# Optimization experiments

Measured on AMD Instinct MI355X. Metric: run time of the kernel, lower is better.

The kernel has to match this reference:

```python
import jax, jax.numpy as jnp
import numpy as np

B, IN, HID, OUT, E, NMAP = 16384, 64, 128, 1, 64, 1000


def setup_inputs() -> dict:
    key = jax.random.key(0)
    ks = jax.random.split(key, 7)
    x = jax.random.normal(ks[0], (B, IN), dtype=jnp.float32)
    num = jax.random.randint(ks[1], (B,), 0, NMAP, dtype=jnp.int64)
    c = jax.random.randint(ks[2], (NMAP,), 0, E, dtype=jnp.int64)
    # per-expert 2-layer MLP params (kaiming-ish scale)
    W1 = jax.random.normal(ks[3], (E, IN, HID), dtype=jnp.float32) * (1.0 / np.sqrt(IN))
    b1 = jnp.zeros((E, HID), dtype=jnp.float32)
    W2 = jax.random.normal(ks[4], (E, HID, OUT), dtype=jnp.float32) * (1.0 / np.sqrt(HID))
    b2 = jnp.zeros((E, OUT), dtype=jnp.float32)
    return {"x": x, "num": num, "c": c, "W1": W1, "b1": b1, "W2": W2, "b2": b2}


def reference(x, num, c, W1, b1, W2, b2):
    # per-sample expert id: c[num[i]]
    e = c[num]                                   # [B]
    # gather each sample's expert weights and run batched MLP
    h = jnp.einsum('bi,bih->bh', x, W1[e]) + b1[e]   # [B, HID]
    h = jax.nn.relu(h)
    y = jnp.einsum('bh,bho->bo', h, W2[e]) + b2[e]   # [B, OUT]
    return jax.nn.sigmoid(y)
```

## Files before the change

kernel.cpp:

```cpp
#include <hip/hip_runtime.h>
#include <math.h>

#define B_N    16384
#define IN_D   64
#define HID_D  128
#define E_N    64
#define SB_N   64
#define CAP_BE 48
#define GRP    4
#define NGRP   (SB_N / GRP)
#define CAPC   (GRP * CAP_BE)

#define FRAG_OFF  0
#define FRAG_SZ   (E_N * IN_D * HID_D * 2)
#define CNT_OFF   (FRAG_OFF + FRAG_SZ)
#define CNT_SZ    (E_N * SB_N * 4)
#define LIST_OFF  (CNT_OFF + CNT_SZ)

typedef __attribute__((ext_vector_type(8))) short v8s;
typedef __attribute__((ext_vector_type(4))) float v4f;

__device__ __forceinline__ short f2bf(float f) {
    unsigned int u = __float_as_uint(f);
    u += 0x7fffu + ((u >> 16) & 1u);
    return (short)(u >> 16);
}

__global__ __launch_bounds__(256) void ka_prep(
    const int* __restrict__ num, const int* __restrict__ c,
    const float* __restrict__ W1, unsigned char* __restrict__ ws)
{
    const int tid = threadIdx.x;
    if (blockIdx.x < SB_N) {
        __shared__ int lcnt[E_N];
        __shared__ int llist[E_N * CAP_BE];
        int* cnt  = (int*)(ws + CNT_OFF);
        int* list = (int*)(ws + LIST_OFF);
        const int b = blockIdx.x;
        if (tid < E_N) lcnt[tid] = 0;
        const int s = b * 256 + tid;
        const int e = c[num[s]];
        __syncthreads();
        int p = atomicAdd(&lcnt[e], 1);
        if (p < CAP_BE) llist[e * CAP_BE + p] = s;
        __syncthreads();
        if (tid < E_N) cnt[tid * SB_N + b] = min(lcnt[tid], CAP_BE);
        for (int j = tid; j < E_N * CAP_BE; j += 256) {
            const int e2 = j / CAP_BE, slot = j - e2 * CAP_BE;
            list[(e2 * SB_N + b) * CAP_BE + slot] = llist[j];
        }
    } else {
        const int e = blockIdx.x - SB_N;
        const float* W1e = W1 + (size_t)e * (IN_D * HID_D);
        const int f0    = tid * 4;
        const int w     = f0 >> 8, nt = (f0 >> 7) & 1, kh = (f0 >> 6) & 1;
        const int quad  = (f0 >> 4) & 3;
        const int hbase = 32 * w + 16 * nt + (f0 & 15);
        v8s t[4];
        #pragma unroll
        for (int j = 0; j < 8; ++j) {
            const float4 v = *(const float4*)&W1e[(32 * kh + 8 * quad + j) * HID_D + hbase];
            t[0][j] = f2bf(v.x); t[1][j] = f2bf(v.y);
            t[2][j] = f2bf(v.z); t[3][j] = f2bf(v.w);
        }
        v8s* frag = (v8s*)(ws + FRAG_OFF) + (size_t)e * (IN_D * HID_D / 8);
        #pragma unroll
        for (int i = 0; i < 4; ++i) frag[f0 + i] = t[i];
    }
}

__global__ __launch_bounds__(256) void kb_compute(
    const float* __restrict__ x,
    const float* __restrict__ b1, const float* __restrict__ W2,
    const float* __restrict__ b2,
    const unsigned char* __restrict__ ws, float* __restrict__ out)
{
    __shared__ int   s_list[CAPC];
    __shared__ float s_yw[4][CAPC];

    const int tid = threadIdx.x;
    const int e   = blockIdx.x & (E_N - 1);
    const int g   = blockIdx.x >> 6;
    const int* cnt  = (const int*)(ws + CNT_OFF);
    const int* list = (const int*)(ws + LIST_OFF);

    const int4 cv = *(const int4*)&cnt[e * SB_N + g * GRP];
    const int  p0 = 0, p1 = cv.x, p2 = cv.x + cv.y, p3 = p2 + cv.z;
    const int  total = p3 + cv.w;
    const int  pfx[GRP] = { p0, p1, p2, p3 };
    const int  cc[GRP]  = { cv.x, cv.y, cv.z, cv.w };

    const int* lsrc = &list[(e * SB_N + g * GRP) * CAP_BE];
    #pragma unroll
    for (int rep = 0; rep < (GRP * CAP_BE + 255) / 256; ++rep) {
        const int j = rep * 256 + tid;
        if (j < GRP * CAP_BE) {
            const int sub = j / CAP_BE, slot = j - sub * CAP_BE;
            if (slot < cc[sub]) s_list[pfx[sub] + slot] = lsrc[j];
        }
    }

    const int wave = __builtin_amdgcn_readfirstlane(tid >> 6);
    const int lane = tid & 63, l16 = lane & 15, quad = lane >> 4;
    const v8s* frag = (const v8s*)(ws + FRAG_OFF) + (size_t)e * (IN_D * HID_D / 8);
    v8s bfrag[2][2];
    #pragma unroll
    for (int nt = 0; nt < 2; ++nt)
        #pragma unroll
        for (int kh = 0; kh < 2; ++kh)
            bfrag[nt][kh] = frag[((wave * 2 + nt) * 2 + kh) * 64 + lane];

    const int   h0   = 32 * wave + l16, h1 = h0 + 16;
    const float b1v0 = b1[e * HID_D + h0], b1v1 = b1[e * HID_D + h1];
    const float w2v0 = W2[e * HID_D + h0], w2v1 = W2[e * HID_D + h1];
    const float b2v  = b2[e];
    __syncthreads();

    const int ntiles = (total + 15) >> 4;
    for (int mt = 0; mt < ntiles; ++mt) {
        const int idx = mt * 16 + l16;
        const int s   = s_list[min(idx, total - 1)];
        const float4* row = (const float4*)(x + (size_t)s * IN_D);

        const float4 f0 = row[2 * quad],     f1 = row[2 * quad + 1];
        const float4 f2 = row[8 + 2 * quad], f3 = row[8 + 2 * quad + 1];
        v8s a0, a1;
        a0[0]=f2bf(f0.x); a0[1]=f2bf(f0.y); a0[2]=f2bf(f0.z); a0[3]=f2bf(f0.w);
        a0[4]=f2bf(f1.x); a0[5]=f2bf(f1.y); a0[6]=f2bf(f1.z); a0[7]=f2bf(f1.w);
        a1[0]=f2bf(f2.x); a1[1]=f2bf(f2.y); a1[2]=f2bf(f2.z); a1[3]=f2bf(f2.w);
        a1[4]=f2bf(f3.x); a1[5]=f2bf(f3.y); a1[6]=f2bf(f3.z); a1[7]=f2bf(f3.w);

        v4f acc0 = {0.f, 0.f, 0.f, 0.f};
        v4f acc1 = {0.f, 0.f, 0.f, 0.f};
        acc0 = __builtin_amdgcn_mfma_f32_16x16x32_bf16(a0, bfrag[0][0], acc0, 0, 0, 0);
        acc0 = __builtin_amdgcn_mfma_f32_16x16x32_bf16(a1, bfrag[0][1], acc0, 0, 0, 0);
        acc1 = __builtin_amdgcn_mfma_f32_16x16x32_bf16(a0, bfrag[1][0], acc1, 0, 0, 0);
        acc1 = __builtin_amdgcn_mfma_f32_16x16x32_bf16(a1, bfrag[1][1], acc1, 0, 0, 0);

        #pragma unroll
        for (int r = 0; r < 4; ++r) {
            float v = fmaxf(acc0[r] + b1v0, 0.f) * w2v0
                    + fmaxf(acc1[r] + b1v1, 0.f) * w2v1;
            v += __shfl_xor(v, 1);
            v += __shfl_xor(v, 2);
            v += __shfl_xor(v, 4);
            v += __shfl_xor(v, 8);
            if (l16 == 0) s_yw[wave][mt * 16 + quad * 4 + r] = v;
        }
    }
    __syncthreads();

    for (int i = tid; i < total; i += 256) {
        const float t = s_yw[0][i] + s_yw[1][i] + s_yw[2][i] + s_yw[3][i] + b2v;
        out[s_list[i]] = 1.0f / (1.0f + expf(-t));
    }
}

extern "C" void kernel_launch(void* const* d_in, const int* in_sizes, int n_in,
                              void* d_out, int out_size, void* d_ws, size_t ws_size,
                              hipStream_t stream)
{
    const float* x   = (const float*)d_in[0];
    const int*   num = (const int*)  d_in[1];
    const int*   c   = (const int*)  d_in[2];
    const float* W1  = (const float*)d_in[3];
    const float* b1  = (const float*)d_in[4];
    const float* W2  = (const float*)d_in[5];
    const float* b2  = (const float*)d_in[6];
    float*       out = (float*)d_out;
    unsigned char* ws = (unsigned char*)d_ws;

    ka_prep   <<<dim3(SB_N + E_N), dim3(256), 0, stream>>>(num, c, W1, ws);
    kb_compute<<<dim3(E_N * NGRP), dim3(256), 0, stream>>>(x, b1, W2, b2, ws, out);
}
```

Baseline: 75.23 us.

## Fuse routing and weight conversion into a single MoE compute kernel

Merges the prep and compute kernels into one launch. Each (expert, group) block scans its 1024-sample slice of num/c, builds its own sample list with shared-memory atomics, and converts that expert's W1 to bf16 MFMA fragments directly in shared memory. This drops the second kernel launch and the workspace round trip. In exchange, every block repeats the routing scan and the W1 conversion (16x redundant per expert) and uses more LDS. Capacity becomes 256 samples per group, and samples past that are silently dropped.

After: 73.94 us. About the same (-1.7%).

```diff
diff --git a/kernel.cpp b/kernel.cpp
--- a/kernel.cpp
+++ b/kernel.cpp
@@ -1,21 +1,14 @@
 #include <hip/hip_runtime.h>
 #include <math.h>
+
 
 #define B_N    16384
 #define IN_D   64
 #define HID_D  128
 #define E_N    64
-#define SB_N   64
-#define CAP_BE 48
-#define GRP    4
-#define NGRP   (SB_N / GRP)
-#define CAPC   (GRP * CAP_BE)
-
-#define FRAG_OFF  0
-#define FRAG_SZ   (E_N * IN_D * HID_D * 2)
-#define CNT_OFF   (FRAG_OFF + FRAG_SZ)
-#define CNT_SZ    (E_N * SB_N * 4)
-#define LIST_OFF  (CNT_OFF + CNT_SZ)
+#define NGRP   16
+#define GRP_S  (B_N / NGRP)
+#define CAPC   256
 
 typedef __attribute__((ext_vector_type(8))) short v8s;
 typedef __attribute__((ext_vector_type(4))) float v4f;
@@ -26,109 +19,81 @@
     return (short)(u >> 16);
 }
 
-__global__ __launch_bounds__(256) void ka_prep(
-    const int* __restrict__ num, const int* __restrict__ c,
-    const float* __restrict__ W1, unsigned char* __restrict__ ws)
+__global__ __launch_bounds__(256) void moe_fused(
+    const float* __restrict__ x, const int* __restrict__ num,
+    const int* __restrict__ c, const float* __restrict__ W1,
+    const float* __restrict__ b1, const float* __restrict__ W2,
+    const float* __restrict__ b2, float* __restrict__ out)
 {
-    const int tid = threadIdx.x;
-    if (blockIdx.x < SB_N) {
-        __shared__ int lcnt[E_N];
-        __shared__ int llist[E_N * CAP_BE];
-        int* cnt  = (int*)(ws + CNT_OFF);
-        int* list = (int*)(ws + LIST_OFF);
-        const int b = blockIdx.x;
-        if (tid < E_N) lcnt[tid] = 0;
-        const int s = b * 256 + tid;
-        const int e = c[num[s]];
-        __syncthreads();
-        int p = atomicAdd(&lcnt[e], 1);
-        if (p < CAP_BE) llist[e * CAP_BE + p] = s;
-        __syncthreads();
-        if (tid < E_N) cnt[tid * SB_N + b] = min(lcnt[tid], CAP_BE);
-        for (int j = tid; j < E_N * CAP_BE; j += 256) {
-            const int e2 = j / CAP_BE, slot = j - e2 * CAP_BE;
-            list[(e2 * SB_N + b) * CAP_BE + slot] = llist[j];
-        }
-    } else {
-        const int e = blockIdx.x - SB_N;
-        const float* W1e = W1 + (size_t)e * (IN_D * HID_D);
-        const int f0    = tid * 4;
-        const int w     = f0 >> 8, nt = (f0 >> 7) & 1, kh = (f0 >> 6) & 1;
-        const int quad  = (f0 >> 4) & 3;
-        const int hbase = 32 * w + 16 * nt + (f0 & 15);
-        v8s t[4];
-        #pragma unroll
-        for (int j = 0; j < 8; ++j) {
-            const float4 v = *(const float4*)&W1e[(32 * kh + 8 * quad + j) * HID_D + hbase];
-            t[0][j] = f2bf(v.x); t[1][j] = f2bf(v.y);
-            t[2][j] = f2bf(v.z); t[3][j] = f2bf(v.w);
-        }
-        v8s* frag = (v8s*)(ws + FRAG_OFF) + (size_t)e * (IN_D * HID_D / 8);
-        #pragma unroll
-        for (int i = 0; i < 4; ++i) frag[f0 + i] = t[i];
-    }
-}
-
-__global__ __launch_bounds__(256) void kb_compute(
-    const float* __restrict__ x,
-    const float* __restrict__ b1, const float* __restrict__ W2,
-    const float* __restrict__ b2,
-    const unsigned char* __restrict__ ws, float* __restrict__ out)
-{
+    __shared__ v8s   s_frag[IN_D * HID_D / 8];
     __shared__ int   s_list[CAPC];
     __shared__ float s_yw[4][CAPC];
+    __shared__ int   s_cnt;
 
     const int tid = threadIdx.x;
     const int e   = blockIdx.x & (E_N - 1);
     const int g   = blockIdx.x >> 6;
-    const int* cnt  = (const int*)(ws + CNT_OFF);
-    const int* list = (const int*)(ws + LIST_OFF);
 
-    const int4 cv = *(const int4*)&cnt[e * SB_N + g * GRP];
-    const int  p0 = 0, p1 = cv.x, p2 = cv.x + cv.y, p3 = p2 + cv.z;
-    const int  total = p3 + cv.w;
-    const int  pfx[GRP] = { p0, p1, p2, p3 };
-    const int  cc[GRP]  = { cv.x, cv.y, cv.z, cv.w };
+    const int  s0 = g * GRP_S + tid * 4;
+    const int4 nv = *(const int4*)&num[s0];
 
-    const int* lsrc = &list[(e * SB_N + g * GRP) * CAP_BE];
+    const int f0    = tid * 4;
+    const int w     = f0 >> 8, nt = (f0 >> 7) & 1, kh = (f0 >> 6) & 1;
+    const int fq    = (f0 >> 4) & 3;
+    const int hbase = 32 * w + 16 * nt + (f0 & 15);
+    const float* W1e = W1 + (size_t)e * (IN_D * HID_D);
+    float4 wv[8];
     #pragma unroll
-    for (int rep = 0; rep < (GRP * CAP_BE + 255) / 256; ++rep) {
-        const int j = rep * 256 + tid;
-        if (j < GRP * CAP_BE) {
-            const int sub = j / CAP_BE, slot = j - sub * CAP_BE;
-            if (slot < cc[sub]) s_list[pfx[sub] + slot] = lsrc[j];
-        }
+    for (int j = 0; j < 8; ++j)
+        wv[j] = *(const float4*)&W1e[(32 * kh + 8 * fq + j) * HID_D + hbase];
+
+    if (tid == 0) s_cnt = 0;
+    __syncthreads();
+
+    const int e0 = c[nv.x], e1 = c[nv.y], e2 = c[nv.z], e3 = c[nv.w];
+    if (e0 == e) { int p = atomicAdd(&s_cnt, 1); if (p < CAPC) s_list[p] = s0;     }
+    if (e1 == e) { int p = atomicAdd(&s_cnt, 1); if (p < CAPC) s_list[p] = s0 + 1; }
+    if (e2 == e) { int p = atomicAdd(&s_cnt, 1); if (p < CAPC) s_list[p] = s0 + 2; }
+    if (e3 == e) { int p = atomicAdd(&s_cnt, 1); if (p < CAPC) s_list[p] = s0 + 3; }
+
+    v8s t[4];
+    #pragma unroll
+    for (int j = 0; j < 8; ++j) {
+        t[0][j] = f2bf(wv[j].x); t[1][j] = f2bf(wv[j].y);
+        t[2][j] = f2bf(wv[j].z); t[3][j] = f2bf(wv[j].w);
     }
+    #pragma unroll
+    for (int i = 0; i < 4; ++i) s_frag[f0 + i] = t[i];
 
     const int wave = __builtin_amdgcn_readfirstlane(tid >> 6);
-    const int lane = tid & 63, l16 = lane & 15, quad = lane >> 4;
-    const v8s* frag = (const v8s*)(ws + FRAG_OFF) + (size_t)e * (IN_D * HID_D / 8);
-    v8s bfrag[2][2];
-    #pragma unroll
-    for (int nt = 0; nt < 2; ++nt)
-        #pragma unroll
-        for (int kh = 0; kh < 2; ++kh)
-            bfrag[nt][kh] = frag[((wave * 2 + nt) * 2 + kh) * 64 + lane];
-
-    const int   h0   = 32 * wave + l16, h1 = h0 + 16;
+    const int lane = tid & 63, l16 = lane & 15, qd = lane >> 4;
+    const int h0   = 32 * wave + l16, h1 = h0 + 16;
     const float b1v0 = b1[e * HID_D + h0], b1v1 = b1[e * HID_D + h1];
     const float w2v0 = W2[e * HID_D + h0], w2v1 = W2[e * HID_D + h1];
     const float b2v  = b2[e];
     __syncthreads();
 
+    v8s bfrag[2][2];
+    #pragma unroll
+    for (int n2 = 0; n2 < 2; ++n2)
+        #pragma unroll
+        for (int k2 = 0; k2 < 2; ++k2)
+            bfrag[n2][k2] = s_frag[((wave * 2 + n2) * 2 + k2) * 64 + lane];
+
+    const int total  = min(s_cnt, CAPC);
     const int ntiles = (total + 15) >> 4;
     for (int mt = 0; mt < ntiles; ++mt) {
         const int idx = mt * 16 + l16;
         const int s   = s_list[min(idx, total - 1)];
         const float4* row = (const float4*)(x + (size_t)s * IN_D);
 
-        const float4 f0 = row[2 * quad],     f1 = row[2 * quad + 1];
-        const float4 f2 = row[8 + 2 * quad], f3 = row[8 + 2 * quad + 1];
+        const float4 r0 = row[2 * qd],     r1 = row[2 * qd + 1];
+        const float4 r2 = row[8 + 2 * qd], r3 = row[8 + 2 * qd + 1];
         v8s a0, a1;
-        a0[0]=f2bf(f0.x); a0[1]=f2bf(f0.y); a0[2]=f2bf(f0.z); a0[3]=f2bf(f0.w);
-        a0[4]=f2bf(f1.x); a0[5]=f2bf(f1.y); a0[6]=f2bf(f1.z); a0[7]=f2bf(f1.w);
-        a1[0]=f2bf(f2.x); a1[1]=f2bf(f2.y); a1[2]=f2bf(f2.z); a1[3]=f2bf(f2.w);
-        a1[4]=f2bf(f3.x); a1[5]=f2bf(f3.y); a1[6]=f2bf(f3.z); a1[7]=f2bf(f3.w);
+        a0[0]=f2bf(r0.x); a0[1]=f2bf(r0.y); a0[2]=f2bf(r0.z); a0[3]=f2bf(r0.w);
+        a0[4]=f2bf(r1.x); a0[5]=f2bf(r1.y); a0[6]=f2bf(r1.z); a0[7]=f2bf(r1.w);
+        a1[0]=f2bf(r2.x); a1[1]=f2bf(r2.y); a1[2]=f2bf(r2.z); a1[3]=f2bf(r2.w);
+        a1[4]=f2bf(r3.x); a1[5]=f2bf(r3.y); a1[6]=f2bf(r3.z); a1[7]=f2bf(r3.w);
 
         v4f acc0 = {0.f, 0.f, 0.f, 0.f};
         v4f acc1 = {0.f, 0.f, 0.f, 0.f};
@@ -145,14 +110,14 @@
             v += __shfl_xor(v, 2);
             v += __shfl_xor(v, 4);
             v += __shfl_xor(v, 8);
-            if (l16 == 0) s_yw[wave][mt * 16 + quad * 4 + r] = v;
+            if (l16 == 0) s_yw[wave][mt * 16 + qd * 4 + r] = v;
         }
     }
     __syncthreads();
 
     for (int i = tid; i < total; i += 256) {
-        const float t = s_yw[0][i] + s_yw[1][i] + s_yw[2][i] + s_yw[3][i] + b2v;
-        out[s_list[i]] = 1.0f / (1.0f + expf(-t));
+        const float tv = s_yw[0][i] + s_yw[1][i] + s_yw[2][i] + s_yw[3][i] + b2v;
+        out[s_list[i]] = 1.0f / (1.0f + expf(-tv));
     }
 }
 
@@ -168,8 +133,7 @@
     const float* W2  = (const float*)d_in[5];
     const float* b2  = (const float*)d_in[6];
     float*       out = (float*)d_out;
-    unsigned char* ws = (unsigned char*)d_ws;
+    (void)d_ws; (void)ws_size;
 
-    ka_prep   <<<dim3(SB_N + E_N), dim3(256), 0, stream>>>(num, c, W1, ws);
-    kb_compute<<<dim3(E_N * NGRP), dim3(256), 0, stream>>>(x, b1, W2, b2, ws, out);
+    moe_fused<<<dim3(E_N * NGRP), dim3(256), 0, stream>>>(x, num, c, W1, b1, W2, b2, out);
 }
```
